# Optimization experiments

Hardware: AMD Instinct MI355X
Metric: run time of the kernel (lower is better)

Reference implementation:

```python
import jax, jax.numpy as jnp
import numpy as np

NL, DM, DI, DS, DC, DTR, NC = 2, 512, 1024, 8, 4, 32, 50
B, CIN, L = 4, 1, 2048


def _layernorm(x, g, b, eps=1e-5):
    mu = jnp.mean(x, axis=-1, keepdims=True)
    var = jnp.mean((x - mu) ** 2, axis=-1, keepdims=True)
    return (x - mu) * jax.lax.rsqrt(var + eps) * g + b


def _selective_scan(u, dt, A, Bm, Cm, D):
    # u, dt: [B,L,DI]; A: [DI,DS]; Bm, Cm: [B,L,DS]; D: [DI]
    dA = jnp.exp(dt[..., None] * A)                       # [B,L,DI,DS]
    dBu = dt[..., None] * Bm[:, :, None, :] * u[..., None]  # [B,L,DI,DS]

    def step(h, inp):
        dA_t, dBu_t, C_t = inp
        h = dA_t * h + dBu_t                              # [B,DI,DS]
        y = jnp.einsum('bdn,bn->bd', h, C_t)
        return h, y

    h0 = jnp.zeros((u.shape[0], A.shape[0], A.shape[1]), u.dtype)
    xs = (dA.transpose(1, 0, 2, 3), dBu.transpose(1, 0, 2, 3), Cm.transpose(1, 0, 2))
    _, ys = jax.lax.scan(step, h0, xs)                    # ys: [L,B,DI]
    return ys.transpose(1, 0, 2) + u * D


def _mamba(x, in_w, conv_w, conv_b, xp_w, dt_w, dt_b, A_log, D, out_w):
    # x: [B,L,DM]
    xz = x @ in_w.T                                       # [B,L,2*DI]
    u, z = jnp.split(xz, 2, axis=-1)
    # depthwise causal conv1d over L
    upad = jnp.pad(u, ((0, 0), (DC - 1, 0), (0, 0)))
    uc = conv_b + sum(upad[:, k:k + u.shape[1], :] * conv_w[:, k] for k in range(DC))
    uc = jax.nn.silu(uc)
    xdbl = uc @ xp_w.T                                    # [B,L,DTR+2*DS]
    dt = xdbl[..., :DTR]
    Bm = xdbl[..., DTR:DTR + DS]
    Cm = xdbl[..., DTR + DS:]
    dt = jax.nn.softplus(dt @ dt_w.T + dt_b)              # [B,L,DI]
    A = -jnp.exp(A_log)
    y = _selective_scan(uc, dt, A, Bm, Cm, D)
    y = y * jax.nn.silu(z)
    return y @ out_w.T                                    # [B,L,DM]


def _forward(x, inp_w, inp_b, norm_g, norm_b, in_w, conv_w, conv_b, xp_w,
             dt_w, dt_b, A_log, Dp, out_w, fnorm_g, fnorm_b, head_w, head_b):
    h = x.transpose(0, 2, 1) @ inp_w.T + inp_b            # [B,L,DM]
    for i in range(NL):
        res = h
        hn = _layernorm(h, norm_g[i], norm_b[i])
        h = res + _mamba(hn, in_w[i], conv_w[i], conv_b[i], xp_w[i],
                         dt_w[i], dt_b[i], A_log[i], Dp[i], out_w[i])
    h = _layernorm(h, fnorm_g, fnorm_b)
    h = jnp.mean(h, axis=1)                               # [B,DM]
    return h @ head_w.T + head_b                          # [B,NC]


def setup_inputs() -> dict:
    key = jax.random.key(0)
    ks = jax.random.split(key, 10)
    f = jnp.float32
    s = 0.02
    x = jax.random.normal(ks[0], (B, CIN, L), f)
    inp_w = jax.random.normal(ks[1], (DM, CIN), f) * s
    inp_b = jnp.zeros((DM,), f)
    norm_g = jnp.ones((NL, DM), f)
    norm_b = jnp.zeros((NL, DM), f)
    in_w = jax.random.normal(ks[2], (NL, 2 * DI, DM), f) * s
    conv_w = jax.random.normal(ks[3], (NL, DI, DC), f) * s
    conv_b = jnp.zeros((NL, DI), f)
    xp_w = jax.random.normal(ks[4], (NL, DTR + 2 * DS, DI), f) * s
    dt_w = jax.random.normal(ks[5], (NL, DI, DTR), f) * s
    dt_b = jax.random.uniform(ks[6], (NL, DI), f, -5.0, -2.0)
    A_log = jnp.log(jnp.broadcast_to(jnp.arange(1, DS + 1, dtype=f), (NL, DI, DS)))
    Dp = jnp.ones((NL, DI), f)
    out_w = jax.random.normal(ks[7], (NL, DM, DI), f) * s
    fnorm_g = jnp.ones((DM,), f)
    fnorm_b = jnp.zeros((DM,), f)
    head_w = jax.random.normal(ks[8], (NC, DM), f) * s
    head_b = jnp.zeros((NC,), f)
    return dict(x=x, inp_w=inp_w, inp_b=inp_b, norm_g=norm_g, norm_b=norm_b,
                in_w=in_w, conv_w=conv_w, conv_b=conv_b, xp_w=xp_w, dt_w=dt_w,
                dt_b=dt_b, A_log=A_log, Dp=Dp, out_w=out_w, fnorm_g=fnorm_g,
                fnorm_b=fnorm_b, head_w=head_w, head_b=head_b)


def reference(x, inp_w, inp_b, norm_g, norm_b, in_w, conv_w, conv_b, xp_w,
              dt_w, dt_b, A_log, Dp, out_w, fnorm_g, fnorm_b, head_w, head_b):
    return _forward(x, inp_w, inp_b, norm_g, norm_b, in_w, conv_w, conv_b, xp_w,
                    dt_w, dt_b, A_log, Dp, out_w, fnorm_g, fnorm_b, head_w, head_b)
```

## Files before the change

### kernel.cpp

```cpp
#include <hip/hip_runtime.h>
#include <hip/hip_bf16.h>
#include <cstddef>

constexpr int NL = 2, DM = 512, DI = 1024, DS = 8, DC = 4, DTR = 32, NC = 50;
constexpr int B = 4, L = 2048;
constexpr int M = B * L;
constexpr int XZW = 2 * DI;
constexpr int XDW = DTR + 2 * DS;
constexpr int NCH = 64, CH = L / NCH;
constexpr int XSK = 8;

typedef __bf16 bf16_t;
typedef bf16_t bf16x8 __attribute__((ext_vector_type(8)));
typedef bf16_t bf16x4 __attribute__((ext_vector_type(4)));
typedef float f32x4 __attribute__((ext_vector_type(4)));

__global__ void embed_k(const float* __restrict__ x, const float* __restrict__ iw,
                        const float* __restrict__ ib, float* __restrict__ h) {
    int idx = blockIdx.x * blockDim.x + threadIdx.x;
    if (idx >= M * DM / 4) return;
    int d4 = idx % (DM / 4);
    int m = idx / (DM / 4);
    float4 w = reinterpret_cast<const float4*>(iw)[d4];
    float4 bb = reinterpret_cast<const float4*>(ib)[d4];
    float xv = x[m];
    float4 r;
    r.x = xv * w.x + bb.x; r.y = xv * w.y + bb.y;
    r.z = xv * w.z + bb.z; r.w = xv * w.w + bb.w;
    reinterpret_cast<float4*>(h)[idx] = r;
}

constexpr int WN1 = NL * XZW * DM / 4;
constexpr int WN2 = NL * XDW * DI / 4;
constexpr int WN3 = NL * DI * DTR / 4;
constexpr int WN4 = NL * DM * DI / 4;
constexpr int WNT = WN1 + WN2 + WN3 + WN4;
__global__ void cvt_ws_k(const float* __restrict__ s1, const float* __restrict__ s2,
                         const float* __restrict__ s3, const float* __restrict__ s4,
                         bf16_t* __restrict__ d1, bf16_t* __restrict__ d2,
                         bf16_t* __restrict__ d3, bf16_t* __restrict__ d4) {
    int i4 = blockIdx.x * 256 + threadIdx.x;
    const float* s; bf16_t* d; int off;
    if (i4 < WN1) { s = s1; d = d1; off = i4; }
    else if (i4 < WN1 + WN2) { s = s2; d = d2; off = i4 - WN1; }
    else if (i4 < WN1 + WN2 + WN3) { s = s3; d = d3; off = i4 - WN1 - WN2; }
    else if (i4 < WNT) { s = s4; d = d4; off = i4 - WN1 - WN2 - WN3; }
    else return;
    float4 f = reinterpret_cast<const float4*>(s)[off];
    bf16x4 v;
    v[0] = (bf16_t)f.x; v[1] = (bf16_t)f.y; v[2] = (bf16_t)f.z; v[3] = (bf16_t)f.w;
    *reinterpret_cast<bf16x4*>(d + (size_t)off * 4) = v;
}

__global__ __launch_bounds__(256) void layernorm_k(const float* __restrict__ in,
                                                   const float* __restrict__ g,
                                                   const float* __restrict__ b,
                                                   bf16_t* __restrict__ out) {
    int row = blockIdx.x;
    const float* x = in + (size_t)row * DM;
    int t = threadIdx.x;
    float v0 = x[t], v1 = x[t + 256];
    float s = v0 + v1, sq = v0 * v0 + v1 * v1;
    for (int o = 32; o > 0; o >>= 1) {
        s += __shfl_down(s, o);
        sq += __shfl_down(sq, o);
    }
    __shared__ float sums[8];
    if ((t & 63) == 0) { sums[t >> 6] = s; sums[4 + (t >> 6)] = sq; }
    __syncthreads();
    float tot = sums[0] + sums[1] + sums[2] + sums[3];
    float totq = sums[4] + sums[5] + sums[6] + sums[7];
    float mu = tot * (1.0f / DM);
    float var = totq * (1.0f / DM) - mu * mu;
    float rs = rsqrtf(var + 1e-5f);
    out[(size_t)row * DM + t]       = (bf16_t)((v0 - mu) * rs * g[t] + b[t]);
    out[(size_t)row * DM + t + 256] = (bf16_t)((v1 - mu) * rs * g[t + 256] + b[t + 256]);
}

template <int BM, int BN, int EPI, typename TC, int SK>
__global__ __launch_bounds__(256) void gemm_mfma(const bf16_t* __restrict__ A, int lda,
                                                 const bf16_t* __restrict__ W, int ldw,
                                                 const float* __restrict__ bias,
                                                 TC* __restrict__ C, int ldc,
                                                 int Nr, int K) {
    constexpr int WM = BM / 2, WN = BN / 2;
    constexpr int FM = WM / 16, FN = WN / 16;
    constexpr int ACH = BM * 32 / (256 * 8);
    constexpr int WCH = BN * 32 / (256 * 8);
    __shared__ bf16_t As[2][BM * 32];
    __shared__ bf16_t Ws[2][BN * 32];

    int tid = threadIdx.x;
    int m0 = blockIdx.y * BM, n0 = blockIdx.x * BN;
    int Ktot = K;
    if constexpr (SK > 1) {
        int s = blockIdx.z;
        Ktot = K / SK;
        A += (size_t)s * Ktot;
        W += (size_t)s * Ktot;
        C += (size_t)s * (size_t)(gridDim.y * BM) * ldc;
    }
    int wave = tid >> 6, lane = tid & 63;
    int wr = wave >> 1, wc = wave & 1;
    int lr = lane & 15, lk = lane >> 4;

    auto load_tile = [&](int k0, bf16x8* ra, bf16x8* rw) {
#pragma unroll
        for (int c = 0; c < ACH; ++c) {
            int e = tid + c * 256;
            int r = e >> 2, g = e & 3;
            ra[c] = *reinterpret_cast<const bf16x8*>(A + (size_t)(m0 + r) * lda + k0 + g * 8);
        }
#pragma unroll
        for (int c = 0; c < WCH; ++c) {
            int e = tid + c * 256;
            int r = e >> 2, g = e & 3;
            bf16x8 z;
#pragma unroll
            for (int q = 0; q < 8; q++) z[q] = (bf16_t)0.0f;
            rw[c] = (n0 + r < Nr)
                ? *reinterpret_cast<const bf16x8*>(W + (size_t)(n0 + r) * ldw + k0 + g * 8)
                : z;
        }
    };
    auto store_tile = [&](const bf16x8* ra, const bf16x8* rw, int buf) {
#pragma unroll
        for (int c = 0; c < ACH; ++c) {
            int e = tid + c * 256;
            int r = e >> 2, g = e & 3;
            int slot = g ^ ((r >> 1) & 3);
            *reinterpret_cast<bf16x8*>(&As[buf][r * 32 + slot * 8]) = ra[c];
        }
#pragma unroll
        for (int c = 0; c < WCH; ++c) {
            int e = tid + c * 256;
            int r = e >> 2, g = e & 3;
            int slot = g ^ ((r >> 1) & 3);
            *reinterpret_cast<bf16x8*>(&Ws[buf][r * 32 + slot * 8]) = rw[c];
        }
    };

    f32x4 acc[FM][FN];
#pragma unroll
    for (int i = 0; i < FM; i++)
#pragma unroll
        for (int j = 0; j < FN; j++)
#pragma unroll
            for (int q = 0; q < 4; q++) acc[i][j][q] = 0.0f;

    bf16x8 pa[ACH], pw[WCH];
    load_tile(0, pa, pw);
    store_tile(pa, pw, 0);
    __syncthreads();

    int nt = Ktot / 32;
    int cur = 0;
    for (int t = 0; t < nt; ++t) {
        bool pf = (t + 1 < nt);
        if (pf) load_tile((t + 1) * 32, pa, pw);

        bf16x8 af[FM], bfr[FN];
#pragma unroll
        for (int mi = 0; mi < FM; mi++) {
            int r = wr * WM + mi * 16 + lr;
            int slot = lk ^ ((r >> 1) & 3);
            af[mi] = *reinterpret_cast<const bf16x8*>(&As[cur][r * 32 + slot * 8]);
        }
#pragma unroll
        for (int ni = 0; ni < FN; ni++) {
            int r = wc * WN + ni * 16 + lr;
            int slot = lk ^ ((r >> 1) & 3);
            bfr[ni] = *reinterpret_cast<const bf16x8*>(&Ws[cur][r * 32 + slot * 8]);
        }
#pragma unroll
        for (int mi = 0; mi < FM; mi++)
#pragma unroll
            for (int ni = 0; ni < FN; ni++)
                acc[mi][ni] = __builtin_amdgcn_mfma_f32_16x16x32_bf16(af[mi], bfr[ni], acc[mi][ni], 0, 0, 0);

        if (pf) {
            store_tile(pa, pw, cur ^ 1);
            __syncthreads();
            cur ^= 1;
        }
    }

#pragma unroll
    for (int mi = 0; mi < FM; mi++) {
#pragma unroll
        for (int ni = 0; ni < FN; ni++) {
            int col = n0 + wc * WN + ni * 16 + lr;
            if (col >= Nr) continue;
#pragma unroll
            for (int i = 0; i < 4; i++) {
                int row = m0 + wr * WM + mi * 16 + lk * 4 + i;
                size_t idx = (size_t)row * ldc + col;
                float v = acc[mi][ni][i];
                if constexpr (EPI == 0) {
                    C[idx] = (TC)v;
                } else if constexpr (EPI == 1) {
                    C[idx] += v;
                } else {
                    float s = v + bias[col];
                    C[idx] = (TC)((s > 20.0f) ? s : __logf(1.0f + __expf(s)));
                }
            }
        }
    }
}

__global__ void xproj_reduce_k(const float* __restrict__ part, float* __restrict__ xdbl,
                               bf16_t* __restrict__ xdt) {
    int idx = blockIdx.x * blockDim.x + threadIdx.x;
    if (idx >= M * XDW) return;
    int m = idx / XDW, j = idx % XDW;
    float s = 0.f;
#pragma unroll
    for (int sp = 0; sp < XSK; sp++) s += part[((size_t)sp * M + m) * 64 + j];
    xdbl[idx] = s;
    if (j < DTR) xdt[(size_t)m * DTR + j] = (bf16_t)s;
}

__global__ __launch_bounds__(256) void conv_silu_k(const bf16_t* __restrict__ xz,
                                                   const float* __restrict__ cw,
                                                   const float* __restrict__ cb,
                                                   bf16_t* __restrict__ uc) {
    int idx = blockIdx.x * blockDim.x + threadIdx.x;
    if (idx >= M * DI / 8) return;
    int d8 = idx % (DI / 8);
    int m = idx / (DI / 8);
    int b = m / L, l = m % L;
    int d0 = d8 * 8;

    float acc[8];
    {
        float4 c0 = *reinterpret_cast<const float4*>(cb + d0);
        float4 c1 = *reinterpret_cast<const float4*>(cb + d0 + 4);
        acc[0] = c0.x; acc[1] = c0.y; acc[2] = c0.z; acc[3] = c0.w;
        acc[4] = c1.x; acc[5] = c1.y; acc[6] = c1.z; acc[7] = c1.w;
    }
    float4 w[8];
#pragma unroll
    for (int j = 0; j < 8; j++)
        w[j] = *reinterpret_cast<const float4*>(cw + (size_t)(d0 + j) * DC);

#pragma unroll
    for (int k = 0; k < DC; k++) {
        int ls = l + k - (DC - 1);
        if (ls < 0) continue;
        bf16x8 v = *reinterpret_cast<const bf16x8*>(xz + (size_t)(b * L + ls) * XZW + d0);
        float wk[8] = {w[0].x, w[1].x, w[2].x, w[3].x, w[4].x, w[5].x, w[6].x, w[7].x};
        if (k == 1) { wk[0]=w[0].y; wk[1]=w[1].y; wk[2]=w[2].y; wk[3]=w[3].y; wk[4]=w[4].y; wk[5]=w[5].y; wk[6]=w[6].y; wk[7]=w[7].y; }
        if (k == 2) { wk[0]=w[0].z; wk[1]=w[1].z; wk[2]=w[2].z; wk[3]=w[3].z; wk[4]=w[4].z; wk[5]=w[5].z; wk[6]=w[6].z; wk[7]=w[7].z; }
        if (k == 3) { wk[0]=w[0].w; wk[1]=w[1].w; wk[2]=w[2].w; wk[3]=w[3].w; wk[4]=w[4].w; wk[5]=w[5].w; wk[6]=w[6].w; wk[7]=w[7].w; }
#pragma unroll
        for (int j = 0; j < 8; j++) acc[j] += (float)v[j] * wk[j];
    }
    bf16x8 o;
#pragma unroll
    for (int j = 0; j < 8; j++) {
        float a = acc[j];
        o[j] = (bf16_t)(a / (1.0f + __expf(-a)));
    }
    *reinterpret_cast<bf16x8*>(uc + (size_t)m * DI + d0) = o;
}

__global__ __launch_bounds__(256) void scan_part_k(const bf16_t* __restrict__ dt,
                                                   const bf16_t* __restrict__ uc,
                                                   const float* __restrict__ xdbl,
                                                   const float* __restrict__ A_log,
                                                   float* __restrict__ hpart,
                                                   float* __restrict__ aprod) {
    int gid = blockIdx.x * 256 + threadIdx.x;
    if (gid >= B * NCH * DI) return;
    int d = gid % DI;
    int c = (gid / DI) % NCH;
    int b = gid / (DI * NCH);
    float Av[DS];
    {
        float4 a0 = *reinterpret_cast<const float4*>(A_log + d * DS);
        float4 a1 = *reinterpret_cast<const float4*>(A_log + d * DS + 4);
        Av[0] = -__expf(a0.x); Av[1] = -__expf(a0.y); Av[2] = -__expf(a0.z); Av[3] = -__expf(a0.w);
        Av[4] = -__expf(a1.x); Av[5] = -__expf(a1.y); Av[6] = -__expf(a1.z); Av[7] = -__expf(a1.w);
    }
    float h[DS] = {};
    float ap[DS];
#pragma unroll
    for (int n = 0; n < DS; n++) ap[n] = 1.0f;
    int l0 = c * CH;
    for (int t = 0; t < CH; t++) {
        size_t row = (size_t)b * L + l0 + t;
        float dtv = (float)dt[row * DI + d];
        float uv = (float)uc[row * DI + d];
        const float4* xr4 = reinterpret_cast<const float4*>(xdbl + row * XDW + DTR);
        float4 b0 = xr4[0], b1 = xr4[1];
        float Bv[DS] = {b0.x, b0.y, b0.z, b0.w, b1.x, b1.y, b1.z, b1.w};
        float du = dtv * uv;
#pragma unroll
        for (int n = 0; n < DS; n++) {
            float dA = __expf(dtv * Av[n]);
            h[n] = dA * h[n] + du * Bv[n];
            ap[n] *= dA;
        }
    }
    size_t base = (((size_t)(b * NCH + c) * DI) + d) * DS;
    f32x4* hp4 = reinterpret_cast<f32x4*>(hpart + base);
    f32x4* ap4 = reinterpret_cast<f32x4*>(aprod + base);
    f32x4 v0, v1, w0, w1;
#pragma unroll
    for (int n = 0; n < 4; n++) { v0[n] = h[n]; v1[n] = h[n + 4]; w0[n] = ap[n]; w1[n] = ap[n + 4]; }
    hp4[0] = v0; hp4[1] = v1;
    ap4[0] = w0; ap4[1] = w1;
}

__global__ void scan_combine_k(float* __restrict__ hpart, const float* __restrict__ aprod) {
    int gid = blockIdx.x * blockDim.x + threadIdx.x;
    if (gid >= B * DI * DS) return;
    int dn = gid & (DI * DS - 1);
    int b = gid >> 13;
    float hrun = 0.f;
    for (int c = 0; c < NCH; c++) {
        size_t idx = ((size_t)(b * NCH + c) * DI * DS) + dn;
        float ap = aprod[idx];
        float hp = hpart[idx];
        hpart[idx] = hrun;
        hrun = ap * hrun + hp;
    }
}

__global__ __launch_bounds__(256) void scan_emit_k(const bf16_t* __restrict__ dt,
                                                   const bf16_t* __restrict__ uc,
                                                   const float* __restrict__ xdbl,
                                                   const bf16_t* __restrict__ xz,
                                                   const float* __restrict__ A_log,
                                                   const float* __restrict__ Dp,
                                                   const float* __restrict__ hpart,
                                                   bf16_t* __restrict__ y) {
    int gid = blockIdx.x * 256 + threadIdx.x;
    if (gid >= B * NCH * DI) return;
    int d = gid % DI;
    int c = (gid / DI) % NCH;
    int b = gid / (DI * NCH);
    float Av[DS];
    {
        float4 a0 = *reinterpret_cast<const float4*>(A_log + d * DS);
        float4 a1 = *reinterpret_cast<const float4*>(A_log + d * DS + 4);
        Av[0] = -__expf(a0.x); Av[1] = -__expf(a0.y); Av[2] = -__expf(a0.z); Av[3] = -__expf(a0.w);
        Av[4] = -__expf(a1.x); Av[5] = -__expf(a1.y); Av[6] = -__expf(a1.z); Av[7] = -__expf(a1.w);
    }
    float h[DS];
    {
        size_t base = (((size_t)(b * NCH + c) * DI) + d) * DS;
        const f32x4* hp4 = reinterpret_cast<const f32x4*>(hpart + base);
        f32x4 v0 = hp4[0], v1 = hp4[1];
#pragma unroll
        for (int n = 0; n < 4; n++) { h[n] = v0[n]; h[n + 4] = v1[n]; }
    }
    float Dv = Dp[d];
    int l0 = c * CH;
    for (int t = 0; t < CH; t++) {
        size_t row = (size_t)b * L + l0 + t;
        float dtv = (float)dt[row * DI + d];
        float uv = (float)uc[row * DI + d];
        const float4* xr4 = reinterpret_cast<const float4*>(xdbl + row * XDW + DTR);
        float4 b0 = xr4[0], b1 = xr4[1], c0 = xr4[2], c1 = xr4[3];
        float Bv[DS] = {b0.x, b0.y, b0.z, b0.w, b1.x, b1.y, b1.z, b1.w};
        float Cv[DS] = {c0.x, c0.y, c0.z, c0.w, c1.x, c1.y, c1.z, c1.w};
        float du = dtv * uv;
        float yv = 0.f;
#pragma unroll
        for (int n = 0; n < DS; n++) {
            float dA = __expf(dtv * Av[n]);
            h[n] = dA * h[n] + du * Bv[n];
            yv += h[n] * Cv[n];
        }
        yv += uv * Dv;
        float zv = (float)xz[row * XZW + DI + d];
        yv *= zv / (1.0f + __expf(-zv));
        y[row * DI + d] = (bf16_t)yv;
    }
}

__global__ __launch_bounds__(256) void mean_part_k(const bf16_t* __restrict__ hn,
                                                   float* __restrict__ partial) {
    int c = blockIdx.x;
    int b = blockIdx.y;
    int t = threadIdx.x;
    int d0 = (t & 63) * 8;
    int rsub = t >> 6;
    float s[8] = {};
    for (int l = rsub; l < 64; l += 4) {
        bf16x8 v = *reinterpret_cast<const bf16x8*>(hn + (size_t)(b * L + c * 64 + l) * DM + d0);
#pragma unroll
        for (int j = 0; j < 8; j++) s[j] += (float)v[j];
    }
    float* dst = partial + ((size_t)(b * 32 + c) * 4 + rsub) * DM + d0;
    f32x4 o0, o1;
#pragma unroll
    for (int j = 0; j < 4; j++) { o0[j] = s[j]; o1[j] = s[j + 4]; }
    reinterpret_cast<f32x4*>(dst)[0] = o0;
    reinterpret_cast<f32x4*>(dst)[1] = o1;
}

__global__ void mean_fin_k(const float* __restrict__ partial, float* __restrict__ hmean) {
    int idx = blockIdx.x * blockDim.x + threadIdx.x;
    if (idx >= B * DM) return;
    int b = idx / DM, d = idx % DM;
    float s = 0.f;
    for (int c = 0; c < 128; c++) s += partial[((size_t)b * 128 + c) * DM + d];
    hmean[idx] = s * (1.0f / L);
}

__global__ void head_k(const float* __restrict__ hmean, const float* __restrict__ hw,
                       const float* __restrict__ hb, float* __restrict__ out) {
    int t = threadIdx.x;
    if (t >= B * NC) return;
    int b = t / NC, c = t % NC;
    float acc = hb[c];
    for (int k = 0; k < DM; k++) acc += hmean[b * DM + k] * hw[c * DM + k];
    out[t] = acc;
}

extern "C" void kernel_launch(void* const* d_in, const int* in_sizes, int n_in,
                              void* d_out, int out_size, void* d_ws, size_t ws_size,
                              hipStream_t stream) {
    const float* x      = (const float*)d_in[0];
    const float* inp_w  = (const float*)d_in[1];
    const float* inp_b  = (const float*)d_in[2];
    const float* norm_g = (const float*)d_in[3];
    const float* norm_b = (const float*)d_in[4];
    const float* in_w   = (const float*)d_in[5];
    const float* conv_w = (const float*)d_in[6];
    const float* conv_b = (const float*)d_in[7];
    const float* xp_w   = (const float*)d_in[8];
    const float* dt_w   = (const float*)d_in[9];
    const float* dt_b   = (const float*)d_in[10];
    const float* A_log  = (const float*)d_in[11];
    const float* Dp     = (const float*)d_in[12];
    const float* out_w  = (const float*)d_in[13];
    const float* fnorm_g = (const float*)d_in[14];
    const float* fnorm_b = (const float*)d_in[15];
    const float* head_w = (const float*)d_in[16];
    const float* head_b = (const float*)d_in[17];
    float* out = (float*)d_out;

    char* p = (char*)d_ws;
    float*  h     = (float*)p;  p += (size_t)M * DM * 4;
    bf16_t* hn    = (bf16_t*)p; p += (size_t)M * DM * 2;
    bf16_t* xz    = (bf16_t*)p; p += (size_t)M * XZW * 2;
    bf16_t* uc    = (bf16_t*)p; p += (size_t)M * DI * 2;
    float*  xdbl  = (float*)p;  p += (size_t)M * XDW * 4;
    bf16_t* xdt   = (bf16_t*)p; p += (size_t)M * DTR * 2;
    bf16_t* dtb   = (bf16_t*)p; p += (size_t)M * DI * 2;
    bf16_t* yb    = (bf16_t*)p; p += (size_t)M * DI * 2;
    float*  hpart = (float*)p;  p += (size_t)B * DI * NCH * DS * 4;
    float*  aprod = (float*)p;  p += (size_t)B * DI * NCH * DS * 4;
    float*  xpart = (float*)p;  p += (size_t)XSK * M * 64 * 4;
    float*  partial = (float*)p; p += (size_t)B * 128 * DM * 4;
    float*  hmean = (float*)p;  p += (size_t)B * DM * 4;
    bf16_t* wb_in = (bf16_t*)p; p += (size_t)NL * XZW * DM * 2;
    bf16_t* wb_xp = (bf16_t*)p; p += (size_t)NL * XDW * DI * 2;
    bf16_t* wb_dt = (bf16_t*)p; p += (size_t)NL * DI * DTR * 2;
    bf16_t* wb_out = (bf16_t*)p; p += (size_t)NL * DM * DI * 2;

    cvt_ws_k<<<(WNT + 255) / 256, 256, 0, stream>>>(in_w, xp_w, dt_w, out_w,
                                                    wb_in, wb_xp, wb_dt, wb_out);
    embed_k<<<(M * DM / 4 + 255) / 256, 256, 0, stream>>>(x, inp_w, inp_b, h);

    for (int i = 0; i < NL; i++) {
        const bf16_t* inw_i = wb_in + (size_t)i * XZW * DM;
        const float* cw_i  = conv_w + (size_t)i * DI * DC;
        const float* cb_i  = conv_b + (size_t)i * DI;
        const bf16_t* xpw_i = wb_xp + (size_t)i * XDW * DI;
        const bf16_t* dtw_i = wb_dt + (size_t)i * DI * DTR;
        const float* dtb_i = dt_b + (size_t)i * DI;
        const float* Al_i  = A_log + (size_t)i * DI * DS;
        const float* Dp_i  = Dp + (size_t)i * DI;
        const bf16_t* ow_i  = wb_out + (size_t)i * DM * DI;

        layernorm_k<<<M, 256, 0, stream>>>(h, norm_g + i * DM, norm_b + i * DM, hn);
        gemm_mfma<128, 64, 0, bf16_t, 1><<<dim3(XZW / 64, M / 128), 256, 0, stream>>>(
            hn, DM, inw_i, DM, nullptr, xz, XZW, XZW, DM);
        conv_silu_k<<<(M * DI / 8 + 255) / 256, 256, 0, stream>>>(xz, cw_i, cb_i, uc);
        gemm_mfma<64, 64, 0, float, XSK><<<dim3(1, M / 64, XSK), 256, 0, stream>>>(
            uc, DI, xpw_i, DI, nullptr, xpart, 64, XDW, DI);
        xproj_reduce_k<<<(M * XDW + 255) / 256, 256, 0, stream>>>(xpart, xdbl, xdt);
        gemm_mfma<64, 64, 2, bf16_t, 1><<<dim3(DI / 64, M / 64), 256, 0, stream>>>(
            xdt, DTR, dtw_i, DTR, dtb_i, dtb, DI, DI, DTR);
        scan_part_k<<<(B * NCH * DI) / 256, 256, 0, stream>>>(dtb, uc, xdbl, Al_i, hpart, aprod);
        scan_combine_k<<<(B * DI * DS + 255) / 256, 256, 0, stream>>>(hpart, aprod);
        scan_emit_k<<<(B * NCH * DI) / 256, 256, 0, stream>>>(dtb, uc, xdbl, xz, Al_i, Dp_i, hpart, yb);
        gemm_mfma<64, 64, 1, float, 1><<<dim3(DM / 64, M / 64), 256, 0, stream>>>(
            yb, DI, ow_i, DI, nullptr, h, DM, DM, DI);
    }

    layernorm_k<<<M, 256, 0, stream>>>(h, fnorm_g, fnorm_b, hn);
    mean_part_k<<<dim3(32, B), 256, 0, stream>>>(hn, partial);
    mean_fin_k<<<(B * DM + 255) / 256, 256, 0, stream>>>(partial, hmean);
    head_k<<<1, 256, 0, stream>>>(hmean, head_w, head_b, out);
}
```

Baseline: 497.7 us.

## Load GEMM tiles directly into LDS, fuse embed with first layernorm, widen in-proj tile

The GEMM staging now uses global_load_lds to copy 16-byte chunks straight from global memory into LDS, with the XOR swizzle applied on the global address side. This removes the register round-trip and the bounds-checked zero fill. Because the bounds check is gone, the x-proj weight is padded to 64 rows with zeros in the conversion kernel. The embedding is fused with the first layer's layernorm, which removes one full pass over h, and the in-proj GEMM tile grows from 128x64 to 128x128. The risks are that LDS-direct loads need correct waitcnt handling before the barrier, and that the larger tile raises register and LDS pressure.

```diff
diff --git a/kernel.cpp b/kernel.cpp
--- a/kernel.cpp
+++ b/kernel.cpp
@@ -7,6 +7,7 @@
 constexpr int M = B * L;
 constexpr int XZW = 2 * DI;
 constexpr int XDW = DTR + 2 * DS;
+constexpr int XPR = 64;
 constexpr int NCH = 64, CH = L / NCH;
 constexpr int XSK = 8;
 
@@ -15,41 +16,86 @@
 typedef bf16_t bf16x4 __attribute__((ext_vector_type(4)));
 typedef float f32x4 __attribute__((ext_vector_type(4)));
 
-__global__ void embed_k(const float* __restrict__ x, const float* __restrict__ iw,
-                        const float* __restrict__ ib, float* __restrict__ h) {
-    int idx = blockIdx.x * blockDim.x + threadIdx.x;
-    if (idx >= M * DM / 4) return;
-    int d4 = idx % (DM / 4);
-    int m = idx / (DM / 4);
-    float4 w = reinterpret_cast<const float4*>(iw)[d4];
-    float4 bb = reinterpret_cast<const float4*>(ib)[d4];
-    float xv = x[m];
-    float4 r;
-    r.x = xv * w.x + bb.x; r.y = xv * w.y + bb.y;
-    r.z = xv * w.z + bb.z; r.w = xv * w.w + bb.w;
-    reinterpret_cast<float4*>(h)[idx] = r;
+__device__ __forceinline__ void gload16(const bf16_t* g, bf16_t* l) {
+    __builtin_amdgcn_global_load_lds(
+        (const __attribute__((address_space(1))) void*)g,
+        (__attribute__((address_space(3))) void*)l, 16, 0, 0);
+}
+
+__global__ __launch_bounds__(256) void embed_ln_k(const float* __restrict__ x,
+                                                  const float* __restrict__ iw,
+                                                  const float* __restrict__ ib,
+                                                  const float* __restrict__ g,
+                                                  const float* __restrict__ bvec,
+                                                  float* __restrict__ h,
+                                                  bf16_t* __restrict__ out) {
+    int row = blockIdx.x;
+    int t = threadIdx.x;
+    float xv = x[row];
+    float v0 = xv * iw[t] + ib[t];
+    float v1 = xv * iw[t + 256] + ib[t + 256];
+    h[(size_t)row * DM + t] = v0;
+    h[(size_t)row * DM + t + 256] = v1;
+    float s = v0 + v1, sq = v0 * v0 + v1 * v1;
+    for (int o = 32; o > 0; o >>= 1) {
+        s += __shfl_down(s, o);
+        sq += __shfl_down(sq, o);
+    }
+    __shared__ float sums[8];
+    if ((t & 63) == 0) { sums[t >> 6] = s; sums[4 + (t >> 6)] = sq; }
+    __syncthreads();
+    float tot = sums[0] + sums[1] + sums[2] + sums[3];
+    float totq = sums[4] + sums[5] + sums[6] + sums[7];
+    float mu = tot * (1.0f / DM);
+    float var = totq * (1.0f / DM) - mu * mu;
+    float rs = rsqrtf(var + 1e-5f);
+    out[(size_t)row * DM + t]       = (bf16_t)((v0 - mu) * rs * g[t] + bvec[t]);
+    out[(size_t)row * DM + t + 256] = (bf16_t)((v1 - mu) * rs * g[t + 256] + bvec[t + 256]);
 }
 
 constexpr int WN1 = NL * XZW * DM / 4;
-constexpr int WN2 = NL * XDW * DI / 4;
+constexpr int WN2p = NL * XPR * DI / 4;
 constexpr int WN3 = NL * DI * DTR / 4;
 constexpr int WN4 = NL * DM * DI / 4;
-constexpr int WNT = WN1 + WN2 + WN3 + WN4;
+constexpr int WNTp = WN1 + WN2p + WN3 + WN4;
 __global__ void cvt_ws_k(const float* __restrict__ s1, const float* __restrict__ s2,
                          const float* __restrict__ s3, const float* __restrict__ s4,
                          bf16_t* __restrict__ d1, bf16_t* __restrict__ d2,
                          bf16_t* __restrict__ d3, bf16_t* __restrict__ d4) {
     int i4 = blockIdx.x * 256 + threadIdx.x;
-    const float* s; bf16_t* d; int off;
-    if (i4 < WN1) { s = s1; d = d1; off = i4; }
-    else if (i4 < WN1 + WN2) { s = s2; d = d2; off = i4 - WN1; }
-    else if (i4 < WN1 + WN2 + WN3) { s = s3; d = d3; off = i4 - WN1 - WN2; }
-    else if (i4 < WNT) { s = s4; d = d4; off = i4 - WN1 - WN2 - WN3; }
-    else return;
-    float4 f = reinterpret_cast<const float4*>(s)[off];
-    bf16x4 v;
-    v[0] = (bf16_t)f.x; v[1] = (bf16_t)f.y; v[2] = (bf16_t)f.z; v[3] = (bf16_t)f.w;
-    *reinterpret_cast<bf16x4*>(d + (size_t)off * 4) = v;
+    if (i4 >= WNTp) return;
+    if (i4 < WN1) {
+        float4 f = reinterpret_cast<const float4*>(s1)[i4];
+        bf16x4 v;
+        v[0] = (bf16_t)f.x; v[1] = (bf16_t)f.y; v[2] = (bf16_t)f.z; v[3] = (bf16_t)f.w;
+        *reinterpret_cast<bf16x4*>(d1 + (size_t)i4 * 4) = v;
+    } else if (i4 < WN1 + WN2p) {
+        int off = i4 - WN1;
+        int layer = off / (XPR * DI / 4);
+        int rem = off % (XPR * DI / 4);
+        int row = rem / (DI / 4);
+        int c4 = rem % (DI / 4);
+        bf16x4 v;
+        if (row < XDW) {
+            float4 f = reinterpret_cast<const float4*>(s2)[((size_t)layer * XDW + row) * (DI / 4) + c4];
+            v[0] = (bf16_t)f.x; v[1] = (bf16_t)f.y; v[2] = (bf16_t)f.z; v[3] = (bf16_t)f.w;
+        } else {
+            v[0] = (bf16_t)0.f; v[1] = (bf16_t)0.f; v[2] = (bf16_t)0.f; v[3] = (bf16_t)0.f;
+        }
+        *reinterpret_cast<bf16x4*>(d2 + (size_t)off * 4) = v;
+    } else if (i4 < WN1 + WN2p + WN3) {
+        int off = i4 - WN1 - WN2p;
+        float4 f = reinterpret_cast<const float4*>(s3)[off];
+        bf16x4 v;
+        v[0] = (bf16_t)f.x; v[1] = (bf16_t)f.y; v[2] = (bf16_t)f.z; v[3] = (bf16_t)f.w;
+        *reinterpret_cast<bf16x4*>(d3 + (size_t)off * 4) = v;
+    } else {
+        int off = i4 - WN1 - WN2p - WN3;
+        float4 f = reinterpret_cast<const float4*>(s4)[off];
+        bf16x4 v;
+        v[0] = (bf16_t)f.x; v[1] = (bf16_t)f.y; v[2] = (bf16_t)f.z; v[3] = (bf16_t)f.w;
+        *reinterpret_cast<bf16x4*>(d4 + (size_t)off * 4) = v;
+    }
 }
 
 __global__ __launch_bounds__(256) void layernorm_k(const float* __restrict__ in,
@@ -85,10 +131,8 @@
                                                  int Nr, int K) {
     constexpr int WM = BM / 2, WN = BN / 2;
     constexpr int FM = WM / 16, FN = WN / 16;
-    constexpr int ACH = BM * 32 / (256 * 8);
-    constexpr int WCH = BN * 32 / (256 * 8);
-    __shared__ bf16_t As[2][BM * 32];
-    __shared__ bf16_t Ws[2][BN * 32];
+    __shared__ __align__(16) bf16_t As[2][BM * 32];
+    __shared__ __align__(16) bf16_t Ws[2][BN * 32];
 
     int tid = threadIdx.x;
     int m0 = blockIdx.y * BM, n0 = blockIdx.x * BN;
@@ -104,41 +148,22 @@
     int wr = wave >> 1, wc = wave & 1;
     int lr = lane & 15, lk = lane >> 4;
 
-    auto load_tile = [&](int k0, bf16x8* ra, bf16x8* rw) {
-#pragma unroll
-        for (int c = 0; c < ACH; ++c) {
+    auto stage = [&](int k0, int buf) {
+#pragma unroll
+        for (int c = 0; c < BM / 64; ++c) {
             int e = tid + c * 256;
-            int r = e >> 2, g = e & 3;
-            ra[c] = *reinterpret_cast<const bf16x8*>(A + (size_t)(m0 + r) * lda + k0 + g * 8);
-        }
-#pragma unroll
-        for (int c = 0; c < WCH; ++c) {
+            int r = e >> 2, slot = e & 3;
+            int g = slot ^ ((r >> 1) & 3);
+            gload16(A + (size_t)(m0 + r) * lda + k0 + g * 8, &As[buf][e * 8]);
+        }
+#pragma unroll
+        for (int c = 0; c < BN / 64; ++c) {
             int e = tid + c * 256;
-            int r = e >> 2, g = e & 3;
-            bf16x8 z;
-#pragma unroll
-            for (int q = 0; q < 8; q++) z[q] = (bf16_t)0.0f;
-            rw[c] = (n0 + r < Nr)
-                ? *reinterpret_cast<const bf16x8*>(W + (size_t)(n0 + r) * ldw + k0 + g * 8)
-                : z;
+            int r = e >> 2, slot = e & 3;
+            int g = slot ^ ((r >> 1) & 3);
+            gload16(W + (size_t)(n0 + r) * ldw + k0 + g * 8, &Ws[buf][e * 8]);
         }
     };
-    auto store_tile = [&](const bf16x8* ra, const bf16x8* rw, int buf) {
-#pragma unroll
-        for (int c = 0; c < ACH; ++c) {
-            int e = tid + c * 256;
-            int r = e >> 2, g = e & 3;
-            int slot = g ^ ((r >> 1) & 3);
-            *reinterpret_cast<bf16x8*>(&As[buf][r * 32 + slot * 8]) = ra[c];
-        }
-#pragma unroll
-        for (int c = 0; c < WCH; ++c) {
-            int e = tid + c * 256;
-            int r = e >> 2, g = e & 3;
-            int slot = g ^ ((r >> 1) & 3);
-            *reinterpret_cast<bf16x8*>(&Ws[buf][r * 32 + slot * 8]) = rw[c];
-        }
-    };
 
     f32x4 acc[FM][FN];
 #pragma unroll
@@ -148,16 +173,13 @@
 #pragma unroll
             for (int q = 0; q < 4; q++) acc[i][j][q] = 0.0f;
 
-    bf16x8 pa[ACH], pw[WCH];
-    load_tile(0, pa, pw);
-    store_tile(pa, pw, 0);
+    stage(0, 0);
     __syncthreads();
 
     int nt = Ktot / 32;
     int cur = 0;
     for (int t = 0; t < nt; ++t) {
-        bool pf = (t + 1 < nt);
-        if (pf) load_tile((t + 1) * 32, pa, pw);
+        if (t + 1 < nt) stage((t + 1) * 32, cur ^ 1);
 
         bf16x8 af[FM], bfr[FN];
 #pragma unroll
@@ -178,11 +200,8 @@
             for (int ni = 0; ni < FN; ni++)
                 acc[mi][ni] = __builtin_amdgcn_mfma_f32_16x16x32_bf16(af[mi], bfr[ni], acc[mi][ni], 0, 0, 0);
 
-        if (pf) {
-            store_tile(pa, pw, cur ^ 1);
-            __syncthreads();
-            cur ^= 1;
-        }
+        __syncthreads();
+        cur ^= 1;
     }
 
 #pragma unroll
@@ -459,27 +478,28 @@
     float*  partial = (float*)p; p += (size_t)B * 128 * DM * 4;
     float*  hmean = (float*)p;  p += (size_t)B * DM * 4;
     bf16_t* wb_in = (bf16_t*)p; p += (size_t)NL * XZW * DM * 2;
-    bf16_t* wb_xp = (bf16_t*)p; p += (size_t)NL * XDW * DI * 2;
+    bf16_t* wb_xp = (bf16_t*)p; p += (size_t)NL * XPR * DI * 2;
     bf16_t* wb_dt = (bf16_t*)p; p += (size_t)NL * DI * DTR * 2;
     bf16_t* wb_out = (bf16_t*)p; p += (size_t)NL * DM * DI * 2;
 
-    cvt_ws_k<<<(WNT + 255) / 256, 256, 0, stream>>>(in_w, xp_w, dt_w, out_w,
-                                                    wb_in, wb_xp, wb_dt, wb_out);
-    embed_k<<<(M * DM / 4 + 255) / 256, 256, 0, stream>>>(x, inp_w, inp_b, h);
+    cvt_ws_k<<<(WNTp + 255) / 256, 256, 0, stream>>>(in_w, xp_w, dt_w, out_w,
+                                                     wb_in, wb_xp, wb_dt, wb_out);
+    embed_ln_k<<<M, 256, 0, stream>>>(x, inp_w, inp_b, norm_g, norm_b, h, hn);
 
     for (int i = 0; i < NL; i++) {
         const bf16_t* inw_i = wb_in + (size_t)i * XZW * DM;
         const float* cw_i  = conv_w + (size_t)i * DI * DC;
         const float* cb_i  = conv_b + (size_t)i * DI;
-        const bf16_t* xpw_i = wb_xp + (size_t)i * XDW * DI;
+        const bf16_t* xpw_i = wb_xp + (size_t)i * XPR * DI;
         const bf16_t* dtw_i = wb_dt + (size_t)i * DI * DTR;
         const float* dtb_i = dt_b + (size_t)i * DI;
         const float* Al_i  = A_log + (size_t)i * DI * DS;
         const float* Dp_i  = Dp + (size_t)i * DI;
         const bf16_t* ow_i  = wb_out + (size_t)i * DM * DI;
 
-        layernorm_k<<<M, 256, 0, stream>>>(h, norm_g + i * DM, norm_b + i * DM, hn);
-        gemm_mfma<128, 64, 0, bf16_t, 1><<<dim3(XZW / 64, M / 128), 256, 0, stream>>>(
+        if (i > 0)
+            layernorm_k<<<M, 256, 0, stream>>>(h, norm_g + i * DM, norm_b + i * DM, hn);
+        gemm_mfma<128, 128, 0, bf16_t, 1><<<dim3(XZW / 128, M / 128), 256, 0, stream>>>(
             hn, DM, inw_i, DM, nullptr, xz, XZW, XZW, DM);
         conv_silu_k<<<(M * DI / 8 + 255) / 256, 256, 0, stream>>>(xz, cw_i, cb_i, uc);
         gemm_mfma<64, 64, 0, float, XSK><<<dim3(1, M / 64, XSK), 256, 0, stream>>>(
```

Measured after the change: 490.8 us. No clear change (-1.4%).
